# Kernel tuning notes

Measured on AMD Instinct MI355X. Metric: run time of the kernel, lower is better.

Reference implementation:

```python
import jax, jax.numpy as jnp
import numpy as np

DIM = 256
HEADS = 8
DIM_HEAD = 64
INNER = HEADS * DIM_HEAD  # 512
SCALE = DIM_HEAD ** -0.5
B, H, W = 8, 64, 64


def setup_inputs() -> dict:
    key = jax.random.key(0)
    ks = jax.random.split(key, 6)
    x = jax.random.normal(ks[0], (B, DIM, H, W), dtype=jnp.float32)
    W_proj = jax.random.normal(ks[1], (DIM, INNER), dtype=jnp.float32) * (DIM ** -0.5)
    step_rep = jax.random.normal(ks[2], (HEADS, 1, 1), dtype=jnp.float32)
    step_x = jax.random.normal(ks[3], (HEADS, 1, 1), dtype=jnp.float32)
    W_out = jax.random.normal(ks[4], (INNER, DIM), dtype=jnp.float32) * (INNER ** -0.5)
    b_out = jax.random.normal(ks[5], (DIM,), dtype=jnp.float32) * 0.01
    return {"x": x, "W_proj": W_proj, "step_rep": step_rep, "step_x": step_x,
            "W_out": W_out, "b_out": b_out}


def _attention(q, k, v):
    # q: [b,h,m,d], k/v: [b,h,n,d]
    dots = jnp.einsum('bhmd,bhnd->bhmn', q, k) * SCALE
    attn = jax.nn.softmax(dots, axis=-1)
    out = jnp.einsum('bhmn,bhnd->bhmd', attn, v)
    return out, attn


def reference(x, W_proj, step_rep, step_x, W_out, b_out):
    b, c, h, w = x.shape
    n = h * w
    # b c h w -> b (h w) c
    x_seq = jnp.transpose(x, (0, 2, 3, 1)).reshape(b, n, c)
    proj = x_seq @ W_proj  # [b, n, inner]
    # AdaptiveAvgPool2d((8,8)) over the (h,w) grid; h,w divisible by 8 -> exact block mean
    proj_2d = proj.reshape(b, h, w, INNER)
    rep = proj_2d.reshape(b, 8, h // 8, 8, w // 8, INNER).mean(axis=(2, 4))  # [b,8,8,inner]
    rep = rep.reshape(b, 64, INNER)
    # split heads
    proj_h = proj.reshape(b, n, HEADS, DIM_HEAD).transpose(0, 2, 1, 3)  # [b,heads,n,dh]
    rep_h = rep.reshape(b, 64, HEADS, DIM_HEAD).transpose(0, 2, 1, 3)   # [b,heads,64,dh]
    # stage 1: 64 pooled queries attend to n keys
    rep_delta, attn = _attention(rep_h, proj_h, proj_h)  # attn: [b,heads,64,n]
    rep2 = rep_h + step_rep * rep_delta
    # stage 2: self-attention among the 64 pooled tokens
    x_delta, _ = _attention(rep2, rep2, rep2)  # [b,heads,64,dh]
    # back-project via attn^T
    x_delta = jnp.einsum('bhmn,bhmd->bhnd', attn, x_delta)  # [b,heads,n,dh]
    x_delta = step_x * x_delta
    # b h n k -> b n (h k)
    x_delta = x_delta.transpose(0, 2, 1, 3).reshape(b, n, INNER)
    x_out = x_delta @ W_out + b_out  # [b, n, dim]
    return x_out.reshape(b, h, w, c).transpose(0, 3, 1, 2)
```

## Files before the change

### kernel.cpp

```cpp
#include <hip/hip_runtime.h>
#include <cstdint>
#include <cstddef>


#define SCALE 0.125f

typedef __attribute__((ext_vector_type(8))) short bf16x8;
typedef __attribute__((ext_vector_type(4))) float f32x4;
typedef __attribute__((ext_vector_type(16))) float f32x16;
typedef __attribute__((ext_vector_type(4))) unsigned int u32x4;

#define MFMA32(a, b, c) __builtin_amdgcn_mfma_f32_32x32x16_bf16(a, b, c, 0, 0, 0)
#define MFMA16(a, b, c) __builtin_amdgcn_mfma_f32_16x16x32_bf16(a, b, c, 0, 0, 0)

__device__ __forceinline__ unsigned short f2bf(float x) {
  unsigned int u = __float_as_uint(x);
  u += 0x7FFFu + ((u >> 16) & 1u);
  return (unsigned short)(u >> 16);
}
__device__ __forceinline__ float bf2f(unsigned short b) {
  return __uint_as_float(((unsigned int)b) << 16);
}
__device__ __forceinline__ void split2(float x, unsigned short& h, unsigned short& l) {
  h = f2bf(x);
  l = f2bf(x - bf2f(h));
}
__device__ __forceinline__ unsigned int cvtpk(float lo, float hi_) {
  unsigned int r;
  asm("v_cvt_pk_bf16_f32 %0, %1, %2" : "=v"(r) : "v"(lo), "v"(hi_));
  return r;
}

typedef const __attribute__((address_space(1))) unsigned int* gas_ptr;
typedef __attribute__((address_space(3))) unsigned int* las_ptr;
__device__ __forceinline__ void gload16(const void* g, void* l) {
  __builtin_amdgcn_global_load_lds((gas_ptr)(size_t)g,
                                   (las_ptr)(unsigned int)(size_t)l, 16, 0, 0);
}

__global__ __launch_bounds__(256) void tsplit(
    const float* __restrict__ in, long long in_bs,
    unsigned short* __restrict__ oh, unsigned short* __restrict__ ol,
    long long o_bs, int R, int C) {
  __shared__ float T[32][33];
  int bz = blockIdx.z;
  const float* ip = in + (size_t)bz * in_bs;
  unsigned short* oph = oh + (size_t)bz * o_bs;
  unsigned short* opl = ol + (size_t)bz * o_bs;
  int c0 = blockIdx.x * 32, r0 = blockIdx.y * 32;
  int t = threadIdx.x;
  int col = t & 31, row8 = t >> 5;
#pragma unroll
  for (int i = 0; i < 4; i++)
    T[row8 + i * 8][col] = ip[(size_t)(r0 + row8 + i * 8) * C + c0 + col];
  __syncthreads();
  int cp = (t & 15) * 2, rr = t >> 4;
#pragma unroll
  for (int i = 0; i < 2; i++) {
    int orow = rr + i * 16;
    float v0 = T[cp][orow], v1 = T[cp + 1][orow];
    unsigned short h0, l0, h1, l1;
    split2(v0, h0, l0);
    split2(v1, h1, l1);
    size_t o = (size_t)(c0 + orow) * R + r0 + cp;
    *(unsigned int*)(oph + o) = (unsigned int)h0 | ((unsigned int)h1 << 16);
    *(unsigned int*)(opl + o) = (unsigned int)l0 | ((unsigned int)l1 << 16);
  }
}

template <bool F32OUT>
__global__ __launch_bounds__(256) void gemm_sb(
    const unsigned short* __restrict__ Ah, const unsigned short* __restrict__ Al,
    long long a_bs,
    const unsigned short* __restrict__ Bh, long long b_bs,
    float* __restrict__ Cf, unsigned short* __restrict__ Ch, long long c_bs,
    int M, int N, int K, const float* __restrict__ bias, int lnx, int lny) {
  __shared__ unsigned short lds[2][3][128][32];
  int id0 = blockIdx.x;
  int cpx = gridDim.x >> 3;
  int id = (id0 & 7) * cpx + (id0 >> 3);
  int bx = id & ((1 << lnx) - 1);
  int by = (id >> lnx) & ((1 << lny) - 1);
  int bz = id >> (lnx + lny);
  int m0 = by * 128, n0 = bx * 128;
  int tid = threadIdx.x;
  int wave = tid >> 6, lane = tid & 63;
  int wr = wave >> 1, wc = wave & 1;

  const unsigned short* src;
  int r0g, sBeg, nS, dArr;
  if (wave == 0) { src = Ah + (size_t)bz * a_bs; r0g = m0; sBeg = 0; nS = 8; dArr = 0; }
  else if (wave == 1) { src = Al + (size_t)bz * a_bs; r0g = m0; sBeg = 0; nS = 8; dArr = 1; }
  else { src = Bh + (size_t)bz * b_bs; r0g = n0; sBeg = (wave - 2) * 4; nS = 4; dArr = 2; }
  int q = lane >> 2;
  int chunk = (lane & 3) ^ ((q >> 1) & 3);
  const unsigned short* srow = src + (size_t)(r0g + q) * K + chunk * 8;

  int g = lane >> 4, fr = lane & 15;
  int slot = (g ^ ((fr >> 1) & 3)) * 8;
  int offA = (wr * 64 + fr) * 32 + slot;
  int offB = 2 * 4096 + (wc * 64 + fr) * 32 + slot;

  f32x4 acc[4][4];
#pragma unroll
  for (int i = 0; i < 4; i++)
#pragma unroll
    for (int j = 0; j < 4; j++)
#pragma unroll
      for (int r = 0; r < 4; r++) acc[i][j][r] = 0.0f;

  int nt = K >> 5;
  for (int s5 = 0; s5 < nS; ++s5) {
    int ss = sBeg + s5;
    gload16(srow + (size_t)(ss * 16) * K, &lds[0][dArr][ss * 16][0]);
  }
  __syncthreads();
  int cur = 0;
  for (int t0 = 0; t0 < nt; ++t0) {
    if (t0 + 1 < nt) {
      int k0 = (t0 + 1) << 5;
      for (int s5 = 0; s5 < nS; ++s5) {
        int ss = sBeg + s5;
        gload16(srow + (size_t)(ss * 16) * K + k0, &lds[cur ^ 1][dArr][ss * 16][0]);
      }
    }
    const unsigned short* bb = &lds[cur][0][0][0];
    bf16x8 af[2][4], bfv[4];
#pragma unroll
    for (int i = 0; i < 4; i++) {
      af[0][i] = *(const bf16x8*)(bb + offA + i * 512);
      af[1][i] = *(const bf16x8*)(bb + 4096 + offA + i * 512);
      bfv[i] = *(const bf16x8*)(bb + offB + i * 512);
    }
#pragma unroll
    for (int i = 0; i < 4; i++)
#pragma unroll
      for (int j = 0; j < 4; j++) {
        acc[i][j] = MFMA16(af[0][i], bfv[j], acc[i][j]);
        acc[i][j] = MFMA16(af[1][i], bfv[j], acc[i][j]);
      }
    __syncthreads();
    cur ^= 1;
  }

  float* eld = (float*)(&lds[0][0][0][0]) + wave * 1088;
  int rr = lane >> 2, cb = (lane & 3) * 16;
#pragma unroll
  for (int i = 0; i < 4; i++) {
#pragma unroll
    for (int j = 0; j < 4; j++)
#pragma unroll
      for (int qd = 0; qd < 4; qd++)
        eld[(g * 4 + qd) * 68 + fr + j * 16] = acc[i][j][qd];
    __syncthreads();
    int mrow = m0 + wr * 64 + i * 16 + rr;
    int ncol = n0 + wc * 64 + cb;
    float4 v0 = *(const float4*)(eld + rr * 68 + cb);
    float4 v1 = *(const float4*)(eld + rr * 68 + cb + 4);
    float4 v2 = *(const float4*)(eld + rr * 68 + cb + 8);
    float4 v3 = *(const float4*)(eld + rr * 68 + cb + 12);
    if (F32OUT) {
      float bi = bias ? bias[mrow] : 0.0f;
      float* Cb = Cf + (size_t)bz * c_bs + (size_t)mrow * N + ncol;
      *(float4*)(Cb + 0) = make_float4(v0.x + bi, v0.y + bi, v0.z + bi, v0.w + bi);
      *(float4*)(Cb + 4) = make_float4(v1.x + bi, v1.y + bi, v1.z + bi, v1.w + bi);
      *(float4*)(Cb + 8) = make_float4(v2.x + bi, v2.y + bi, v2.z + bi, v2.w + bi);
      *(float4*)(Cb + 12) = make_float4(v3.x + bi, v3.y + bi, v3.z + bi, v3.w + bi);
    } else {
      float vv[16] = {v0.x, v0.y, v0.z, v0.w, v1.x, v1.y, v1.z, v1.w,
                      v2.x, v2.y, v2.z, v2.w, v3.x, v3.y, v3.z, v3.w};
      bf16x8 p0, p1;
#pragma unroll
      for (int k = 0; k < 8; k++) {
        p0[k] = (short)f2bf(vv[k]);
        p1[k] = (short)f2bf(vv[8 + k]);
      }
      unsigned short* Cb = Ch + (size_t)bz * c_bs + (size_t)mrow * N + ncol;
      *(bf16x8*)(Cb + 0) = p0;
      *(bf16x8*)(Cb + 8) = p1;
    }
    __syncthreads();
  }
}

__global__ __launch_bounds__(256) void tpool(
    const unsigned short* __restrict__ projh,
    unsigned short* __restrict__ projTh,
    unsigned short* __restrict__ reph, unsigned short* __restrict__ repl) {
  __shared__ unsigned short Lh[64][64];
  int it = blockIdx.x, py = blockIdx.y, b = blockIdx.z;
  int t = threadIdx.x;
  int ch = t & 63, seg = t >> 6;
  int swc = ((ch ^ (ch >> 3)) & 7) << 3;
  float poolacc[2] = {0.0f, 0.0f};

  for (int dy = 0; dy < 8; dy++) {
    int base_n = py * 512 + dy * 64;
    {
      int rl = t >> 3, cq = (t & 7) * 8;
#pragma unroll
      for (int p = 0; p < 2; p++) {
        int row = rl + p * 32;
        size_t ga = ((size_t)(b * 4096 + base_n + row)) * 512 + it * 64 + cq;
        bf16x8 vh = *(const bf16x8*)(projh + ga);
#pragma unroll
        for (int j = 0; j < 8; j++) {
          int cl = cq + j;
          int sw = ((cl ^ (cl >> 3)) & 7) << 3;
          Lh[cl][row ^ sw] = (unsigned short)vh[j];
        }
      }
    }
    __syncthreads();
#pragma unroll
    for (int half = 0; half < 2; half++) {
      int n0 = seg * 16 + half * 8;
      int n0x = n0 ^ swc;
      bf16x8 rh = *(const bf16x8*)&Lh[ch][n0x];
      size_t o = ((size_t)(b * 512 + it * 64 + ch)) * 4096 + base_n + n0;
      *(bf16x8*)(projTh + o) = rh;
      float ssum = 0.0f;
#pragma unroll
      for (int j = 0; j < 8; j++) ssum += bf2f((unsigned short)rh[j]);
      poolacc[half] += ssum;
    }
    __syncthreads();
  }
#pragma unroll
  for (int half = 0; half < 2; half++) {
    float v = poolacc[half] * 0.015625f;
    unsigned short hh, ll;
    split2(v, hh, ll);
    size_t ro = ((size_t)(b * 64 + py * 8 + seg * 2 + half)) * 512 + it * 64 + ch;
    reph[ro] = hh;
    repl[ro] = ll;
  }
}

__global__ __launch_bounds__(256) void fattn(
    const unsigned short* __restrict__ projh,
    const unsigned short* __restrict__ reph, const unsigned short* __restrict__ repl,
    const unsigned short* __restrict__ projTh,
    unsigned short* __restrict__ PTh,
    float* __restrict__ pvpart, float* __restrict__ lpart) {
  int bh = blockIdx.x, s = blockIdx.y;
  int b = bh >> 3, h = bh & 7;
  int t = threadIdx.x;
  int wave = t >> 6, lane = t & 63;
  int lm = lane & 31, hi = lane >> 5;

  bf16x8 qf[2][4][2];
#pragma unroll
  for (int mt = 0; mt < 2; mt++)
#pragma unroll
    for (int ks = 0; ks < 4; ks++) {
      size_t qo = ((size_t)(b * 64 + mt * 32 + lm)) * 512 + h * 64 + ks * 16 + hi * 8;
      qf[mt][ks][0] = *(const bf16x8*)(reph + qo);
      qf[mt][ks][1] = *(const bf16x8*)(repl + qo);
    }

  f32x16 pv[2][2];
#pragma unroll
  for (int a = 0; a < 2; a++)
#pragma unroll
    for (int c = 0; c < 2; c++)
#pragma unroll
      for (int r = 0; r < 16; r++) pv[a][c][r] = 0.0f;
  float lsum0 = 0.0f, lsum1 = 0.0f;

  for (int sti = 0; sti < 2; sti++) {
    int n0 = s * 512 + (wave * 2 + sti) * 64;
#pragma unroll
    for (int nn = 0; nn < 64; nn += 32) {
      int nb = n0 + nn;
      f32x16 sa0, sa1;
#pragma unroll
      for (int r = 0; r < 16; r++) { sa0[r] = 0.0f; sa1[r] = 0.0f; }
      __builtin_amdgcn_s_setprio(1);
#pragma unroll
      for (int ks = 0; ks < 4; ks++) {
        size_t ko = ((size_t)(b * 4096 + nb + lm)) * 512 + h * 64 + ks * 16 + hi * 8;
        bf16x8 kh = *(const bf16x8*)(projh + ko);
        sa0 = MFMA32(kh, qf[0][ks][0], sa0);
        sa0 = MFMA32(kh, qf[0][ks][1], sa0);
        sa1 = MFMA32(kh, qf[1][ks][0], sa1);
        sa1 = MFMA32(kh, qf[1][ks][1], sa1);
      }
      __builtin_amdgcn_s_setprio(0);
#pragma unroll
      for (int r = 0; r < 16; r++) {
        sa0[r] = __expf(sa0[r] * SCALE); lsum0 += sa0[r];
        sa1[r] = __expf(sa1[r] * SCALE); lsum1 += sa1[r];
      }
      {
        int kk0 = h * 64 + lm, kk1 = kk0 + 32;
#pragma unroll
        for (int r = 0; r < 16; r++) {
          int n = nb + (r & 3) + 8 * (r >> 2) + 4 * hi;
          size_t o = ((size_t)(b * 4096 + n)) * 512;
          PTh[o + kk0] = f2bf(sa0[r]);
          PTh[o + kk1] = f2bf(sa1[r]);
        }
      }
#pragma unroll
      for (int kc = 0; kc < 2; kc++) {
        bf16x8 paH[2], paL[2];
#pragma unroll
        for (int mt = 0; mt < 2; mt++) {
          float pq[8], lq[8];
#pragma unroll
          for (int qi = 0; qi < 8; qi++) {
            float v = (mt == 0) ? sa0[kc * 8 + qi] : sa1[kc * 8 + qi];
            unsigned short ph_ = f2bf(v);
            pq[qi] = v;
            lq[qi] = v - bf2f(ph_);
          }
          int c01 = (int)cvtpk(pq[0], pq[1]), c23 = (int)cvtpk(pq[2], pq[3]);
          int c45 = (int)cvtpk(pq[4], pq[5]), c67 = (int)cvtpk(pq[6], pq[7]);
          int d01 = __shfl_xor(c01, 32), d23 = __shfl_xor(c23, 32);
          int d45 = __shfl_xor(c45, 32), d67 = __shfl_xor(c67, 32);
          u32x4 wv;
          wv.x = (unsigned int)(hi ? d45 : c01);
          wv.y = (unsigned int)(hi ? d67 : c23);
          wv.z = (unsigned int)(hi ? c45 : d01);
          wv.w = (unsigned int)(hi ? c67 : d23);
          paH[mt] = __builtin_bit_cast(bf16x8, wv);
          int e01 = (int)cvtpk(lq[0], lq[1]), e23 = (int)cvtpk(lq[2], lq[3]);
          int e45 = (int)cvtpk(lq[4], lq[5]), e67 = (int)cvtpk(lq[6], lq[7]);
          int f01 = __shfl_xor(e01, 32), f23 = __shfl_xor(e23, 32);
          int f45 = __shfl_xor(e45, 32), f67 = __shfl_xor(e67, 32);
          u32x4 lv;
          lv.x = (unsigned int)(hi ? f45 : e01);
          lv.y = (unsigned int)(hi ? f67 : e23);
          lv.z = (unsigned int)(hi ? e45 : f01);
          lv.w = (unsigned int)(hi ? e67 : f23);
          paL[mt] = __builtin_bit_cast(bf16x8, lv);
        }
#pragma unroll
        for (int dt = 0; dt < 2; dt++) {
          size_t vto = ((size_t)(b * 512 + h * 64 + dt * 32 + lm)) * 4096 +
                       nb + kc * 16 + hi * 8;
          bf16x8 vh = *(const bf16x8*)(projTh + vto);
          __builtin_amdgcn_s_setprio(1);
          pv[0][dt] = MFMA32(paH[0], vh, pv[0][dt]);
          pv[0][dt] = MFMA32(paL[0], vh, pv[0][dt]);
          pv[1][dt] = MFMA32(paH[1], vh, pv[1][dt]);
          pv[1][dt] = MFMA32(paL[1], vh, pv[1][dt]);
          __builtin_amdgcn_s_setprio(0);
        }
      }
    }
  }
  lsum0 += __shfl_xor(lsum0, 32);
  lsum1 += __shfl_xor(lsum1, 32);
  __shared__ float pvbuf[64][64];
  __shared__ float lbuf[4][64];
  if (hi == 0) { lbuf[wave][lm] = lsum0; lbuf[wave][32 + lm] = lsum1; }
  for (int w = 0; w < 4; w++) {
    __syncthreads();
    if (wave == w) {
#pragma unroll
      for (int mt = 0; mt < 2; mt++)
#pragma unroll
        for (int dt = 0; dt < 2; dt++)
#pragma unroll
          for (int r = 0; r < 16; r++) {
            int m = mt * 32 + (r & 3) + 8 * (r >> 2) + 4 * hi;
            int d = dt * 32 + lm;
            if (w == 0) pvbuf[m][d] = pv[mt][dt][r];
            else pvbuf[m][d] += pv[mt][dt][r];
          }
    }
  }
  __syncthreads();
  size_t base = ((size_t)(s * 64 + bh)) * 4096;
  for (int idx = t; idx < 4096; idx += 256)
    pvpart[base + idx] = pvbuf[idx >> 6][idx & 63];
  if (t < 64)
    lpart[((size_t)(s * 64 + bh)) * 64 + t] =
        lbuf[0][t] + lbuf[1][t] + lbuf[2][t] + lbuf[3][t];
}

__global__ __launch_bounds__(256) void stage2f(
    const float* __restrict__ pvpart, const float* __restrict__ lpart,
    const unsigned short* __restrict__ reph, const unsigned short* __restrict__ repl,
    const float* __restrict__ step_rep, const float* __restrict__ step_x,
    const float* __restrict__ Wo,
    unsigned short* __restrict__ GTh, unsigned short* __restrict__ GTl) {
  __shared__ float T[64][68];
  __shared__ float P[64][68];
  __shared__ float Wl[64][68];
  __shared__ float lt[64];
  int bh = blockIdx.x, h = bh & 7, b = bh >> 3;
  int t = threadIdx.x;
  float sr = step_rep[h];
  if (t < 64) {
    float L = 0.0f;
#pragma unroll
    for (int ss = 0; ss < 8; ss++) L += lpart[((size_t)(ss * 64 + bh)) * 64 + t];
    lt[t] = 1.0f / L;
  }
  __syncthreads();
  for (int idx = t; idx < 4096; idx += 256) {
    int m = idx >> 6, d = idx & 63;
    float sum = 0.0f;
#pragma unroll
    for (int ss = 0; ss < 8; ss++)
      sum += pvpart[((size_t)(ss * 64 + bh)) * 4096 + idx];
    size_t ro = ((size_t)(b * 64 + m)) * 512 + h * 64 + d;
    float repv = bf2f(reph[ro]) + bf2f(repl[ro]);
    T[d][m] = repv + sr * sum * lt[m];
  }
  __syncthreads();
  int tx = t & 15, ty = t >> 4;
  {
    float acc[4][4] = {};
#pragma unroll
    for (int k = 0; k < 64; k++) {
      float4 a = *(const float4*)&T[k][ty * 4];
      float4 bv = *(const float4*)&T[k][tx * 4];
      float aa[4] = {a.x, a.y, a.z, a.w};
      float bb[4] = {bv.x, bv.y, bv.z, bv.w};
#pragma unroll
      for (int i = 0; i < 4; i++)
#pragma unroll
        for (int j = 0; j < 4; j++) acc[i][j] += aa[i] * bb[j];
    }
#pragma unroll
    for (int i = 0; i < 4; i++)
      *(float4*)&P[ty * 4 + i][tx * 4] =
          make_float4(acc[i][0] * SCALE, acc[i][1] * SCALE, acc[i][2] * SCALE,
                      acc[i][3] * SCALE);
  }
  __syncthreads();
  if (t < 64) {
    float mx = -3.4e38f;
    for (int n = 0; n < 64; n++) mx = fmaxf(mx, P[t][n]);
    float s = 0.0f;
    for (int n = 0; n < 64; n++) {
      float e = __expf(P[t][n] - mx);
      P[t][n] = e;
      s += e;
    }
    float r = 1.0f / s;
    for (int n = 0; n < 64; n++) P[t][n] *= r;
  }
  __syncthreads();
  float xacc[4][4] = {};
#pragma unroll
  for (int k = 0; k < 64; k++) {
    float aa[4], bb[4];
#pragma unroll
    for (int i = 0; i < 4; i++) {
      aa[i] = P[ty * 4 + i][k];
      bb[i] = T[tx * 4 + i][k];
    }
#pragma unroll
    for (int i = 0; i < 4; i++)
#pragma unroll
      for (int j = 0; j < 4; j++) xacc[i][j] += aa[i] * bb[j];
  }
  __syncthreads();
#pragma unroll
  for (int i = 0; i < 4; i++)
    *(float4*)&P[ty * 4 + i][tx * 4] =
        make_float4(xacc[i][0], xacc[i][1], xacc[i][2], xacc[i][3]);
  float sxh = step_x[h];
  float li[4];
#pragma unroll
  for (int i = 0; i < 4; i++) li[i] = lt[ty * 4 + i] * sxh;
  int wk = t >> 2, wcq = (t & 3) * 16;
  for (int cb = 0; cb < 4; cb++) {
    __syncthreads();
#pragma unroll
    for (int j = 0; j < 4; j++)
      *(float4*)&Wl[wk][wcq + j * 4] =
          *(const float4*)(Wo + ((size_t)(h * 64 + wk)) * 256 + cb * 64 + wcq + j * 4);
    __syncthreads();
    float gacc[4][4] = {};
#pragma unroll
    for (int k = 0; k < 64; k++) {
      float aa[4];
#pragma unroll
      for (int i = 0; i < 4; i++) aa[i] = P[ty * 4 + i][k];
      float4 bv = *(const float4*)&Wl[k][tx * 4];
      float bb[4] = {bv.x, bv.y, bv.z, bv.w};
#pragma unroll
      for (int i = 0; i < 4; i++)
#pragma unroll
        for (int j = 0; j < 4; j++) gacc[i][j] += aa[i] * bb[j];
    }
#pragma unroll
    for (int i = 0; i < 4; i++)
#pragma unroll
      for (int j = 0; j < 4; j++) {
        float val = gacc[i][j] * li[i];
        size_t o = ((size_t)(b * 256 + cb * 64 + tx * 4 + j)) * 512 + h * 64 + ty * 4 + i;
        unsigned short hh, ll;
        split2(val, hh, ll);
        GTh[o] = hh;
        GTl[o] = ll;
      }
  }
}

extern "C" void kernel_launch(void* const* d_in, const int* in_sizes, int n_in,
                              void* d_out, int out_size, void* d_ws, size_t ws_size,
                              hipStream_t stream) {
  const float* x = (const float*)d_in[0];
  const float* Wp = (const float*)d_in[1];
  const float* srep = (const float*)d_in[2];
  const float* sx = (const float*)d_in[3];
  const float* Wo = (const float*)d_in[4];
  const float* bo = (const float*)d_in[5];
  float* out = (float*)d_out;

  char* wsb = (char*)d_ws;
  unsigned short* projh  = (unsigned short*)(wsb + 0);
  unsigned short* projTh = (unsigned short*)(wsb + 33554432);
  unsigned short* xTh    = (unsigned short*)(wsb + 67108864);
  unsigned short* xTl    = (unsigned short*)(wsb + 83886080);
  unsigned short* PTh    = (unsigned short*)(wsb + 67108864);
  unsigned short* WpTh   = (unsigned short*)(wsb + 100663296);
  unsigned short* WpTl   = (unsigned short*)(wsb + 100925440);
  unsigned short* reph   = (unsigned short*)(wsb + 101187584);
  unsigned short* repl   = (unsigned short*)(wsb + 101711872);
  float* pvpart          = (float*)(wsb + 102236160);
  float* lpart           = (float*)(wsb + 110624768);
  unsigned short* GTh    = (unsigned short*)(wsb + 110755840);
  unsigned short* GTl    = (unsigned short*)(wsb + 112852992);

  tsplit<<<dim3(128, 8, 8), 256, 0, stream>>>(x, (long long)256 * 4096,
                                              xTh, xTl, (long long)4096 * 256, 256, 4096);
  tsplit<<<dim3(16, 8, 1), 256, 0, stream>>>(Wp, 0, WpTh, WpTl, 0, 256, 512);
  gemm_sb<false><<<dim3(1024), 256, 0, stream>>>(
      xTh, xTl, (long long)4096 * 256, WpTh, 0,
      nullptr, projh, (long long)4096 * 512, 4096, 512, 256, nullptr, 2, 5);
  tpool<<<dim3(8, 8, 8), 256, 0, stream>>>(projh, projTh, reph, repl);
  fattn<<<dim3(64, 8), 256, 0, stream>>>(projh, reph, repl, projTh, PTh,
                                         pvpart, lpart);
  stage2f<<<dim3(64), 256, 0, stream>>>(pvpart, lpart, reph, repl, srep, sx,
                                        Wo, GTh, GTl);
  gemm_sb<true><<<dim3(512), 256, 0, stream>>>(
      GTh, GTl, (long long)256 * 512, PTh, (long long)4096 * 512,
      out, nullptr, (long long)256 * 4096, 256, 4096, 512, bo, 5, 1);
}
```

Before: 231.2 us.

## Drop bf16 split-precision in GEMMs, merge transposes, re-split attention across waves

```diff
diff --git a/kernel.cpp b/kernel.cpp
--- a/kernel.cpp
+++ b/kernel.cpp
@@ -38,15 +38,25 @@
                                    (las_ptr)(unsigned int)(size_t)l, 16, 0, 0);
 }
 
-__global__ __launch_bounds__(256) void tsplit(
-    const float* __restrict__ in, long long in_bs,
-    unsigned short* __restrict__ oh, unsigned short* __restrict__ ol,
-    long long o_bs, int R, int C) {
+__global__ __launch_bounds__(256) void tsplit9(
+    const float* __restrict__ x, const float* __restrict__ Wp,
+    unsigned short* __restrict__ xTh, unsigned short* __restrict__ WpTh) {
   __shared__ float T[32][33];
-  int bz = blockIdx.z;
-  const float* ip = in + (size_t)bz * in_bs;
-  unsigned short* oph = oh + (size_t)bz * o_bs;
-  unsigned short* opl = ol + (size_t)bz * o_bs;
+  int z = blockIdx.z;
+  const float* ip;
+  unsigned short* oph;
+  int C;
+  const int R = 256;
+  if (z < 8) {
+    ip = x + (size_t)z * 256 * 4096;
+    oph = xTh + (size_t)z * 4096 * 256;
+    C = 4096;
+  } else {
+    if (blockIdx.x >= 16) return;
+    ip = Wp;
+    oph = WpTh;
+    C = 512;
+  }
   int c0 = blockIdx.x * 32, r0 = blockIdx.y * 32;
   int t = threadIdx.x;
   int col = t & 31, row8 = t >> 5;
@@ -58,107 +68,111 @@
 #pragma unroll
   for (int i = 0; i < 2; i++) {
     int orow = rr + i * 16;
-    float v0 = T[cp][orow], v1 = T[cp + 1][orow];
-    unsigned short h0, l0, h1, l1;
-    split2(v0, h0, l0);
-    split2(v1, h1, l1);
+    unsigned short h0 = f2bf(T[cp][orow]);
+    unsigned short h1 = f2bf(T[cp + 1][orow]);
     size_t o = (size_t)(c0 + orow) * R + r0 + cp;
     *(unsigned int*)(oph + o) = (unsigned int)h0 | ((unsigned int)h1 << 16);
-    *(unsigned int*)(opl + o) = (unsigned int)l0 | ((unsigned int)l1 << 16);
-  }
-}
-
-template <bool F32OUT>
-__global__ __launch_bounds__(256) void gemm_sb(
-    const unsigned short* __restrict__ Ah, const unsigned short* __restrict__ Al,
-    long long a_bs,
+  }
+}
+
+template <int BM, bool F32OUT>
+__global__ __launch_bounds__(256) void gemm_1t(
+    const unsigned short* __restrict__ Ah, long long a_bs,
     const unsigned short* __restrict__ Bh, long long b_bs,
     float* __restrict__ Cf, unsigned short* __restrict__ Ch, long long c_bs,
     int M, int N, int K, const float* __restrict__ bias, int lnx, int lny) {
-  __shared__ unsigned short lds[2][3][128][32];
+  constexpr int ROWS = BM + 128;
+  __shared__ unsigned short lds[2][ROWS * 32];
   int id0 = blockIdx.x;
   int cpx = gridDim.x >> 3;
   int id = (id0 & 7) * cpx + (id0 >> 3);
   int bx = id & ((1 << lnx) - 1);
   int by = (id >> lnx) & ((1 << lny) - 1);
   int bz = id >> (lnx + lny);
-  int m0 = by * 128, n0 = bx * 128;
+  int m0 = by * BM, n0 = bx * 128;
   int tid = threadIdx.x;
   int wave = tid >> 6, lane = tid & 63;
   int wr = wave >> 1, wc = wave & 1;
 
-  const unsigned short* src;
-  int r0g, sBeg, nS, dArr;
-  if (wave == 0) { src = Ah + (size_t)bz * a_bs; r0g = m0; sBeg = 0; nS = 8; dArr = 0; }
-  else if (wave == 1) { src = Al + (size_t)bz * a_bs; r0g = m0; sBeg = 0; nS = 8; dArr = 1; }
-  else { src = Bh + (size_t)bz * b_bs; r0g = n0; sBeg = (wave - 2) * 4; nS = 4; dArr = 2; }
+  const unsigned short* Ab = Ah + (size_t)bz * a_bs;
+  const unsigned short* Bb = Bh + (size_t)bz * b_bs;
   int q = lane >> 2;
   int chunk = (lane & 3) ^ ((q >> 1) & 3);
-  const unsigned short* srow = src + (size_t)(r0g + q) * K + chunk * 8;
+
+  constexpr int ASL = BM / 16;
+  constexpr int TOT = ASL + 8;
+  int sl0 = wave * TOT / 4, myN = (wave + 1) * TOT / 4 - wave * TOT / 4;
+  const unsigned short* sSrc[4];
+  unsigned sLds[4];
+  for (int i = 0; i < 4; ++i) {
+    int sl = sl0 + i;
+    if (i < myN) {
+      if (sl < ASL) {
+        sSrc[i] = Ab + (size_t)(m0 + sl * 16 + q) * K + chunk * 8;
+        sLds[i] = (unsigned)(sl * 16) * 32;
+      } else {
+        int bs = sl - ASL;
+        sSrc[i] = Bb + (size_t)(n0 + bs * 16 + q) * K + chunk * 8;
+        sLds[i] = (unsigned)(BM + bs * 16) * 32;
+      }
+    } else {
+      sSrc[i] = nullptr;
+      sLds[i] = 0;
+    }
+  }
 
   int g = lane >> 4, fr = lane & 15;
   int slot = (g ^ ((fr >> 1) & 3)) * 8;
-  int offA = (wr * 64 + fr) * 32 + slot;
-  int offB = 2 * 4096 + (wc * 64 + fr) * 32 + slot;
-
-  f32x4 acc[4][4];
-#pragma unroll
-  for (int i = 0; i < 4; i++)
+  int offA = (wr * (BM / 2) + fr) * 32 + slot;
+  int offB = (BM + wc * 64 + fr) * 32 + slot;
+
+  constexpr int MI = BM / 32;
+  f32x4 acc[MI][4];
+#pragma unroll
+  for (int i = 0; i < MI; i++)
 #pragma unroll
     for (int j = 0; j < 4; j++)
 #pragma unroll
       for (int r = 0; r < 4; r++) acc[i][j][r] = 0.0f;
 
   int nt = K >> 5;
-  for (int s5 = 0; s5 < nS; ++s5) {
-    int ss = sBeg + s5;
-    gload16(srow + (size_t)(ss * 16) * K, &lds[0][dArr][ss * 16][0]);
-  }
+  for (int i = 0; i < myN; ++i) gload16(sSrc[i], &lds[0][sLds[i]]);
   __syncthreads();
   int cur = 0;
   for (int t0 = 0; t0 < nt; ++t0) {
     if (t0 + 1 < nt) {
       int k0 = (t0 + 1) << 5;
-      for (int s5 = 0; s5 < nS; ++s5) {
-        int ss = sBeg + s5;
-        gload16(srow + (size_t)(ss * 16) * K + k0, &lds[cur ^ 1][dArr][ss * 16][0]);
-      }
-    }
-    const unsigned short* bb = &lds[cur][0][0][0];
-    bf16x8 af[2][4], bfv[4];
-#pragma unroll
-    for (int i = 0; i < 4; i++) {
-      af[0][i] = *(const bf16x8*)(bb + offA + i * 512);
-      af[1][i] = *(const bf16x8*)(bb + 4096 + offA + i * 512);
-      bfv[i] = *(const bf16x8*)(bb + offB + i * 512);
-    }
-#pragma unroll
-    for (int i = 0; i < 4; i++)
-#pragma unroll
-      for (int j = 0; j < 4; j++) {
-        acc[i][j] = MFMA16(af[0][i], bfv[j], acc[i][j]);
-        acc[i][j] = MFMA16(af[1][i], bfv[j], acc[i][j]);
-      }
+      for (int i = 0; i < myN; ++i)
+        gload16(sSrc[i] + k0, &lds[cur ^ 1][sLds[i]]);
+    }
+    bf16x8 af[MI], bfv[4];
+#pragma unroll
+    for (int i = 0; i < MI; i++) af[i] = *(const bf16x8*)(&lds[cur][offA + i * 512]);
+#pragma unroll
+    for (int j = 0; j < 4; j++) bfv[j] = *(const bf16x8*)(&lds[cur][offB + j * 512]);
+#pragma unroll
+    for (int i = 0; i < MI; i++)
+#pragma unroll
+      for (int j = 0; j < 4; j++) acc[i][j] = MFMA16(af[i], bfv[j], acc[i][j]);
     __syncthreads();
     cur ^= 1;
   }
 
-  float* eld = (float*)(&lds[0][0][0][0]) + wave * 1088;
-  int rr = lane >> 2, cb = (lane & 3) * 16;
-#pragma unroll
-  for (int i = 0; i < 4; i++) {
+  float* eld = (float*)(&lds[0][0]) + wave * 1088;
+  int rr2 = lane >> 2, cb2 = (lane & 3) * 16;
+#pragma unroll
+  for (int i = 0; i < MI; i++) {
 #pragma unroll
     for (int j = 0; j < 4; j++)
 #pragma unroll
       for (int qd = 0; qd < 4; qd++)
         eld[(g * 4 + qd) * 68 + fr + j * 16] = acc[i][j][qd];
-    __syncthreads();
-    int mrow = m0 + wr * 64 + i * 16 + rr;
-    int ncol = n0 + wc * 64 + cb;
-    float4 v0 = *(const float4*)(eld + rr * 68 + cb);
-    float4 v1 = *(const float4*)(eld + rr * 68 + cb + 4);
-    float4 v2 = *(const float4*)(eld + rr * 68 + cb + 8);
-    float4 v3 = *(const float4*)(eld + rr * 68 + cb + 12);
+    int mrow = m0 + wr * (BM / 2) + i * 16 + rr2;
+    int ncol = n0 + wc * 64 + cb2;
+    float4 v0 = *(const float4*)(eld + rr2 * 68 + cb2);
+    float4 v1 = *(const float4*)(eld + rr2 * 68 + cb2 + 4);
+    float4 v2 = *(const float4*)(eld + rr2 * 68 + cb2 + 8);
+    float4 v3 = *(const float4*)(eld + rr2 * 68 + cb2 + 12);
     if (F32OUT) {
       float bi = bias ? bias[mrow] : 0.0f;
       float* Cb = Cf + (size_t)bz * c_bs + (size_t)mrow * N + ncol;
@@ -237,7 +251,7 @@
   }
 }
 
-__global__ __launch_bounds__(256) void fattn(
+__global__ __launch_bounds__(256, 4) void fattn(
     const unsigned short* __restrict__ projh,
     const unsigned short* __restrict__ reph, const unsigned short* __restrict__ repl,
     const unsigned short* __restrict__ projTh,
@@ -248,145 +262,130 @@
   int t = threadIdx.x;
   int wave = t >> 6, lane = t & 63;
   int lm = lane & 31, hi = lane >> 5;
-
-  bf16x8 qf[2][4][2];
-#pragma unroll
-  for (int mt = 0; mt < 2; mt++)
+  int mt = wave & 1, kh = wave >> 1;
+
+  bf16x8 qf[4][2];
+#pragma unroll
+  for (int ks = 0; ks < 4; ks++) {
+    size_t qo = ((size_t)(b * 64 + mt * 32 + lm)) * 512 + h * 64 + ks * 16 + hi * 8;
+    qf[ks][0] = *(const bf16x8*)(reph + qo);
+    qf[ks][1] = *(const bf16x8*)(repl + qo);
+  }
+
+  f32x16 pv[2];
+#pragma unroll
+  for (int c = 0; c < 2; c++)
+#pragma unroll
+    for (int r = 0; r < 16; r++) pv[c][r] = 0.0f;
+  float lsum = 0.0f;
+
+  int n0 = s * 256 + kh * 128;
+#pragma unroll
+  for (int c4 = 0; c4 < 4; c4++) {
+    int nb = n0 + c4 * 32;
+    f32x16 sa;
+#pragma unroll
+    for (int r = 0; r < 16; r++) sa[r] = 0.0f;
+    __builtin_amdgcn_s_setprio(1);
 #pragma unroll
     for (int ks = 0; ks < 4; ks++) {
-      size_t qo = ((size_t)(b * 64 + mt * 32 + lm)) * 512 + h * 64 + ks * 16 + hi * 8;
-      qf[mt][ks][0] = *(const bf16x8*)(reph + qo);
-      qf[mt][ks][1] = *(const bf16x8*)(repl + qo);
-    }
-
-  f32x16 pv[2][2];
-#pragma unroll
-  for (int a = 0; a < 2; a++)
-#pragma unroll
-    for (int c = 0; c < 2; c++)
-#pragma unroll
-      for (int r = 0; r < 16; r++) pv[a][c][r] = 0.0f;
-  float lsum0 = 0.0f, lsum1 = 0.0f;
-
-  for (int sti = 0; sti < 2; sti++) {
-    int n0 = s * 512 + (wave * 2 + sti) * 64;
-#pragma unroll
-    for (int nn = 0; nn < 64; nn += 32) {
-      int nb = n0 + nn;
-      f32x16 sa0, sa1;
-#pragma unroll
-      for (int r = 0; r < 16; r++) { sa0[r] = 0.0f; sa1[r] = 0.0f; }
-      __builtin_amdgcn_s_setprio(1);
-#pragma unroll
-      for (int ks = 0; ks < 4; ks++) {
-        size_t ko = ((size_t)(b * 4096 + nb + lm)) * 512 + h * 64 + ks * 16 + hi * 8;
-        bf16x8 kh = *(const bf16x8*)(projh + ko);
-        sa0 = MFMA32(kh, qf[0][ks][0], sa0);
-        sa0 = MFMA32(kh, qf[0][ks][1], sa0);
-        sa1 = MFMA32(kh, qf[1][ks][0], sa1);
-        sa1 = MFMA32(kh, qf[1][ks][1], sa1);
-      }
-      __builtin_amdgcn_s_setprio(0);
+      size_t ko = ((size_t)(b * 4096 + nb + lm)) * 512 + h * 64 + ks * 16 + hi * 8;
+      bf16x8 kh8 = *(const bf16x8*)(projh + ko);
+      sa = MFMA32(kh8, qf[ks][0], sa);
+      sa = MFMA32(kh8, qf[ks][1], sa);
+    }
+    __builtin_amdgcn_s_setprio(0);
+#pragma unroll
+    for (int r = 0; r < 16; r++) {
+      sa[r] = __expf(sa[r] * SCALE);
+      lsum += sa[r];
+    }
+    {
+      int kk = h * 64 + mt * 32 + lm;
 #pragma unroll
       for (int r = 0; r < 16; r++) {
-        sa0[r] = __expf(sa0[r] * SCALE); lsum0 += sa0[r];
-        sa1[r] = __expf(sa1[r] * SCALE); lsum1 += sa1[r];
-      }
+        int n = nb + (r & 3) + 8 * (r >> 2) + 4 * hi;
+        PTh[((size_t)(b * 4096 + n)) * 512 + kk] = f2bf(sa[r]);
+      }
+    }
+#pragma unroll
+    for (int kc = 0; kc < 2; kc++) {
+      bf16x8 paH, paL;
       {
-        int kk0 = h * 64 + lm, kk1 = kk0 + 32;
+        float pq[8], lq[8];
+#pragma unroll
+        for (int qi = 0; qi < 8; qi++) {
+          float v = sa[kc * 8 + qi];
+          unsigned short ph_ = f2bf(v);
+          pq[qi] = v;
+          lq[qi] = v - bf2f(ph_);
+        }
+        int c01 = (int)cvtpk(pq[0], pq[1]), c23 = (int)cvtpk(pq[2], pq[3]);
+        int c45 = (int)cvtpk(pq[4], pq[5]), c67 = (int)cvtpk(pq[6], pq[7]);
+        int d01 = __shfl_xor(c01, 32), d23 = __shfl_xor(c23, 32);
+        int d45 = __shfl_xor(c45, 32), d67 = __shfl_xor(c67, 32);
+        u32x4 wv;
+        wv.x = (unsigned int)(hi ? d45 : c01);
+        wv.y = (unsigned int)(hi ? d67 : c23);
+        wv.z = (unsigned int)(hi ? c45 : d01);
+        wv.w = (unsigned int)(hi ? c67 : d23);
+        paH = __builtin_bit_cast(bf16x8, wv);
+        int e01 = (int)cvtpk(lq[0], lq[1]), e23 = (int)cvtpk(lq[2], lq[3]);
+        int e45 = (int)cvtpk(lq[4], lq[5]), e67 = (int)cvtpk(lq[6], lq[7]);
+        int f01 = __shfl_xor(e01, 32), f23 = __shfl_xor(e23, 32);
+        int f45 = __shfl_xor(e45, 32), f67 = __shfl_xor(e67, 32);
+        u32x4 lv;
+        lv.x = (unsigned int)(hi ? f45 : e01);
+        lv.y = (unsigned int)(hi ? f67 : e23);
+        lv.z = (unsigned int)(hi ? e45 : f01);
+        lv.w = (unsigned int)(hi ? e67 : f23);
+        paL = __builtin_bit_cast(bf16x8, lv);
+      }
+#pragma unroll
+      for (int dt = 0; dt < 2; dt++) {
+        size_t vto = ((size_t)(b * 512 + h * 64 + dt * 32 + lm)) * 4096 +
+                     nb + kc * 16 + hi * 8;
+        bf16x8 vh = *(const bf16x8*)(projTh + vto);
+        __builtin_amdgcn_s_setprio(1);
+        pv[dt] = MFMA32(paH, vh, pv[dt]);
+        pv[dt] = MFMA32(paL, vh, pv[dt]);
+        __builtin_amdgcn_s_setprio(0);
+      }
+    }
+  }
+  lsum += __shfl_xor(lsum, 32);
+  __shared__ float pvbuf[64][64];
+  __shared__ float lbuf[4][32];
+  if (hi == 0) lbuf[wave][lm] = lsum;
+  for (int w = 0; w < 4; w++) {
+    __syncthreads();
+    if (wave == w) {
+#pragma unroll
+      for (int dt = 0; dt < 2; dt++)
 #pragma unroll
         for (int r = 0; r < 16; r++) {
-          int n = nb + (r & 3) + 8 * (r >> 2) + 4 * hi;
-          size_t o = ((size_t)(b * 4096 + n)) * 512;
-          PTh[o + kk0] = f2bf(sa0[r]);
-          PTh[o + kk1] = f2bf(sa1[r]);
+          int m = mt * 32 + (r & 3) + 8 * (r >> 2) + 4 * hi;
+          int d = dt * 32 + lm;
+          if (w < 2) pvbuf[m][d] = pv[dt][r];
+          else pvbuf[m][d] += pv[dt][r];
         }
-      }
-#pragma unroll
-      for (int kc = 0; kc < 2; kc++) {
-        bf16x8 paH[2], paL[2];
-#pragma unroll
-        for (int mt = 0; mt < 2; mt++) {
-          float pq[8], lq[8];
-#pragma unroll
-          for (int qi = 0; qi < 8; qi++) {
-            float v = (mt == 0) ? sa0[kc * 8 + qi] : sa1[kc * 8 + qi];
-            unsigned short ph_ = f2bf(v);
-            pq[qi] = v;
-            lq[qi] = v - bf2f(ph_);
-          }
-          int c01 = (int)cvtpk(pq[0], pq[1]), c23 = (int)cvtpk(pq[2], pq[3]);
-          int c45 = (int)cvtpk(pq[4], pq[5]), c67 = (int)cvtpk(pq[6], pq[7]);
-          int d01 = __shfl_xor(c01, 32), d23 = __shfl_xor(c23, 32);
-          int d45 = __shfl_xor(c45, 32), d67 = __shfl_xor(c67, 32);
-          u32x4 wv;
-          wv.x = (unsigned int)(hi ? d45 : c01);
-          wv.y = (unsigned int)(hi ? d67 : c23);
-          wv.z = (unsigned int)(hi ? c45 : d01);
-          wv.w = (unsigned int)(hi ? c67 : d23);
-          paH[mt] = __builtin_bit_cast(bf16x8, wv);
-          int e01 = (int)cvtpk(lq[0], lq[1]), e23 = (int)cvtpk(lq[2], lq[3]);
-          int e45 = (int)cvtpk(lq[4], lq[5]), e67 = (int)cvtpk(lq[6], lq[7]);
-          int f01 = __shfl_xor(e01, 32), f23 = __shfl_xor(e23, 32);
-          int f45 = __shfl_xor(e45, 32), f67 = __shfl_xor(e67, 32);
-          u32x4 lv;
-          lv.x = (unsigned int)(hi ? f45 : e01);
-          lv.y = (unsigned int)(hi ? f67 : e23);
-          lv.z = (unsigned int)(hi ? e45 : f01);
-          lv.w = (unsigned int)(hi ? e67 : f23);
-          paL[mt] = __builtin_bit_cast(bf16x8, lv);
-        }
-#pragma unroll
-        for (int dt = 0; dt < 2; dt++) {
-          size_t vto = ((size_t)(b * 512 + h * 64 + dt * 32 + lm)) * 4096 +
-                       nb + kc * 16 + hi * 8;
-          bf16x8 vh = *(const bf16x8*)(projTh + vto);
-          __builtin_amdgcn_s_setprio(1);
-          pv[0][dt] = MFMA32(paH[0], vh, pv[0][dt]);
-          pv[0][dt] = MFMA32(paL[0], vh, pv[0][dt]);
-          pv[1][dt] = MFMA32(paH[1], vh, pv[1][dt]);
-          pv[1][dt] = MFMA32(paL[1], vh, pv[1][dt]);
-          __builtin_amdgcn_s_setprio(0);
-        }
-      }
-    }
-  }
-  lsum0 += __shfl_xor(lsum0, 32);
-  lsum1 += __shfl_xor(lsum1, 32);
-  __shared__ float pvbuf[64][64];
-  __shared__ float lbuf[4][64];
-  if (hi == 0) { lbuf[wave][lm] = lsum0; lbuf[wave][32 + lm] = lsum1; }
-  for (int w = 0; w < 4; w++) {
-    __syncthreads();
-    if (wave == w) {
-#pragma unroll
-      for (int mt = 0; mt < 2; mt++)
-#pragma unroll
-        for (int dt = 0; dt < 2; dt++)
-#pragma unroll
-          for (int r = 0; r < 16; r++) {
-            int m = mt * 32 + (r & 3) + 8 * (r >> 2) + 4 * hi;
-            int d = dt * 32 + lm;
-            if (w == 0) pvbuf[m][d] = pv[mt][dt][r];
-            else pvbuf[m][d] += pv[mt][dt][r];
-          }
     }
   }
   __syncthreads();
   size_t base = ((size_t)(s * 64 + bh)) * 4096;
   for (int idx = t; idx < 4096; idx += 256)
     pvpart[base + idx] = pvbuf[idx >> 6][idx & 63];
-  if (t < 64)
-    lpart[((size_t)(s * 64 + bh)) * 64 + t] =
-        lbuf[0][t] + lbuf[1][t] + lbuf[2][t] + lbuf[3][t];
+  if (t < 64) {
+    int mt2 = t >> 5, lm2 = t & 31;
+    lpart[((size_t)(s * 64 + bh)) * 64 + t] = lbuf[mt2][lm2] + lbuf[2 + mt2][lm2];
+  }
 }
 
 __global__ __launch_bounds__(256) void stage2f(
     const float* __restrict__ pvpart, const float* __restrict__ lpart,
     const unsigned short* __restrict__ reph, const unsigned short* __restrict__ repl,
     const float* __restrict__ step_rep, const float* __restrict__ step_x,
-    const float* __restrict__ Wo,
-    unsigned short* __restrict__ GTh, unsigned short* __restrict__ GTl) {
+    const float* __restrict__ Wo, unsigned short* __restrict__ GTh) {
   __shared__ float T[64][68];
   __shared__ float P[64][68];
   __shared__ float Wl[64][68];
@@ -397,7 +396,7 @@
   if (t < 64) {
     float L = 0.0f;
 #pragma unroll
-    for (int ss = 0; ss < 8; ss++) L += lpart[((size_t)(ss * 64 + bh)) * 64 + t];
+    for (int ss = 0; ss < 16; ss++) L += lpart[((size_t)(ss * 64 + bh)) * 64 + t];
     lt[t] = 1.0f / L;
   }
   __syncthreads();
@@ -405,7 +404,7 @@
     int m = idx >> 6, d = idx & 63;
     float sum = 0.0f;
 #pragma unroll
-    for (int ss = 0; ss < 8; ss++)
+    for (int ss = 0; ss < 16; ss++)
       sum += pvpart[((size_t)(ss * 64 + bh)) * 4096 + idx];
     size_t ro = ((size_t)(b * 64 + m)) * 512 + h * 64 + d;
     float repv = bf2f(reph[ro]) + bf2f(repl[ro]);
@@ -496,10 +495,7 @@
       for (int j = 0; j < 4; j++) {
         float val = gacc[i][j] * li[i];
         size_t o = ((size_t)(b * 256 + cb * 64 + tx * 4 + j)) * 512 + h * 64 + ty * 4 + i;
-        unsigned short hh, ll;
-        split2(val, hh, ll);
-        GTh[o] = hh;
-        GTl[o] = ll;
+        GTh[o] = f2bf(val);
       }
   }
 }
@@ -519,29 +515,24 @@
   unsigned short* projh  = (unsigned short*)(wsb + 0);
   unsigned short* projTh = (unsigned short*)(wsb + 33554432);
   unsigned short* xTh    = (unsigned short*)(wsb + 67108864);
-  unsigned short* xTl    = (unsigned short*)(wsb + 83886080);
   unsigned short* PTh    = (unsigned short*)(wsb + 67108864);
   unsigned short* WpTh   = (unsigned short*)(wsb + 100663296);
-  unsigned short* WpTl   = (unsigned short*)(wsb + 100925440);
-  unsigned short* reph   = (unsigned short*)(wsb + 101187584);
-  unsigned short* repl   = (unsigned short*)(wsb + 101711872);
-  float* pvpart          = (float*)(wsb + 102236160);
-  float* lpart           = (float*)(wsb + 110624768);
-  unsigned short* GTh    = (unsigned short*)(wsb + 110755840);
-  unsigned short* GTl    = (unsigned short*)(wsb + 112852992);
-
-  tsplit<<<dim3(128, 8, 8), 256, 0, stream>>>(x, (long long)256 * 4096,
-                                              xTh, xTl, (long long)4096 * 256, 256, 4096);
-  tsplit<<<dim3(16, 8, 1), 256, 0, stream>>>(Wp, 0, WpTh, WpTl, 0, 256, 512);
-  gemm_sb<false><<<dim3(1024), 256, 0, stream>>>(
-      xTh, xTl, (long long)4096 * 256, WpTh, 0,
+  unsigned short* reph   = (unsigned short*)(wsb + 100925440);
+  unsigned short* repl   = (unsigned short*)(wsb + 101449728);
+  float* pvpart          = (float*)(wsb + 101974016);
+  float* lpart           = (float*)(wsb + 118751232);
+  unsigned short* GTh    = (unsigned short*)(wsb + 119013376);
+
+  tsplit9<<<dim3(128, 8, 9), 256, 0, stream>>>(x, Wp, xTh, WpTh);
+  gemm_1t<128, false><<<dim3(1024), 256, 0, stream>>>(
+      xTh, (long long)4096 * 256, WpTh, 0,
       nullptr, projh, (long long)4096 * 512, 4096, 512, 256, nullptr, 2, 5);
   tpool<<<dim3(8, 8, 8), 256, 0, stream>>>(projh, projTh, reph, repl);
-  fattn<<<dim3(64, 8), 256, 0, stream>>>(projh, reph, repl, projTh, PTh,
-                                         pvpart, lpart);
+  fattn<<<dim3(64, 16), 256, 0, stream>>>(projh, reph, repl, projTh, PTh,
+                                          pvpart, lpart);
   stage2f<<<dim3(64), 256, 0, stream>>>(pvpart, lpart, reph, repl, srep, sx,
-                                        Wo, GTh, GTl);
-  gemm_sb<true><<<dim3(512), 256, 0, stream>>>(
-      GTh, GTl, (long long)256 * 512, PTh, (long long)4096 * 512,
-      out, nullptr, (long long)256 * 4096, 256, 4096, 512, bo, 5, 1);
-}
+                                        Wo, GTh);
+  gemm_1t<64, true><<<dim3(1024), 256, 0, stream>>>(
+      GTh, (long long)256 * 512, PTh, (long long)4096 * 512,
+      out, nullptr, (long long)256 * 4096, 256, 4096, 512, bo, 5, 2);
+}
```

Result: faster. 211.5 us (-8.5%).
